# Kernel tuning notes

Measured on AMD Instinct MI355X. Metric: run time of the kernel, lower is better.

Reference implementation:

```python
import jax, jax.numpy as jnp
import numpy as np

GAIN_CAP = 0.99
EPS = 1e-4


def _clamp(v):
    # clamp_preserve_grad(v, 0.0, cap) == cap - relu(cap - relu(v))
    r = jax.nn.relu
    return GAIN_CAP - r(GAIN_CAP - r(v))


def _pos(p):
    return jax.nn.softplus(p) + EPS


def setup_inputs() -> dict:
    key = jax.random.key(0)
    ks = jax.random.split(key, 12)
    B, C, H, W, O, M = 4, 128, 256, 256, 16, 32
    return {
        "x": jax.random.normal(ks[0], (B, C, H, W), jnp.float32),
        "steer": jax.random.normal(ks[1], (B, O, H, W), jnp.float32),
        "modulation": jax.random.normal(ks[2], (B, M), jnp.float32),
        "r_center": 0.1 * jax.random.normal(ks[3], (C,), jnp.float32),
        "r_horizontal": 0.1 * jax.random.normal(ks[4], (C,), jnp.float32),
        "r_vertical": 0.1 * jax.random.normal(ks[5], (C,), jnp.float32),
        "r_diag": 0.1 * jax.random.normal(ks[6], (C,), jnp.float32),
        "gain_horizontal": 0.1 * jax.random.normal(ks[7], (C,), jnp.float32),
        "gain_vertical": 0.1 * jax.random.normal(ks[8], (C,), jnp.float32),
        "gain_diag": 0.1 * jax.random.normal(ks[9], (C,), jnp.float32),
        "steer_w": 0.1 * jax.random.normal(ks[10], (4, O), jnp.float32),  # 1x1 conv weight squeezed
        "mod_w": 0.1 * jax.random.normal(ks[11], (3, M), jnp.float32),    # Linear(M,3,bias=False)
    }


def reference(x, steer, modulation, r_center, r_horizontal, r_vertical, r_diag,
              gain_horizontal, gain_vertical, gain_diag, steer_w, mod_w):
    cview = lambda p: p[None, :, None, None]  # (1,C,1,1)
    center = x
    right = jnp.roll(x, -1, axis=-1)
    left = jnp.roll(x, 1, axis=-1)
    up = jnp.roll(x, 1, axis=-2)
    down = jnp.roll(x, -1, axis=-2)
    diag_ne = jnp.roll(x, (-1, -1), axis=(-2, -1))
    diag_sw = jnp.roll(x, (1, 1), axis=(-2, -1))
    diag_nw = jnp.roll(x, (1, -1), axis=(-2, -1))
    diag_se = jnp.roll(x, (-1, 1), axis=(-2, -1))

    r_c = cview(_pos(r_center))
    r_h = cview(_pos(r_horizontal))
    r_v = cview(_pos(r_vertical))
    r_d = cview(_pos(r_diag))

    flow_h = (right - center + (left - center)) / (r_c + r_h)
    flow_v = (up - center + (down - center)) / (r_c + r_v)
    flow_d = (diag_ne - center + (diag_sw - center) + (diag_nw - center) + (diag_se - center)) / (2.0 * (r_c + r_d))

    gh = jnp.tanh(cview(gain_horizontal))
    gv = jnp.tanh(cview(gain_vertical))
    gd = jnp.tanh(cview(gain_diag))

    # modulation gating: [B,3] -> [B,3,1,1]
    delta = jnp.tanh(modulation @ mod_w.T)[:, :, None, None]
    gh = _clamp(gh * (1.0 + 0.1 * delta[:, 0:1]))
    gv = _clamp(gv * (1.0 + 0.1 * delta[:, 1:2]))
    gd = _clamp(gd * (1.0 + 0.1 * delta[:, 2:3]))

    # steer gating: 1x1 conv (no bias) then tanh -> [B,4,H,W]
    steer_fields = jnp.tanh(jnp.einsum('bohw,po->bphw', steer, steer_w))
    gh = _clamp(gh * (1.0 + 0.2 * steer_fields[:, 0:1]))
    gv = _clamp(gv * (1.0 + 0.2 * steer_fields[:, 1:2]))
    gd = _clamp(gd * (1.0 + 0.2 * steer_fields[:, 2:3]))

    update = gh * flow_h + gv * flow_v + gd * flow_d
    return center + update
```

## Files before the change

### kernel.cpp

```cpp
#include <hip/hip_runtime.h>
#include <math.h>

#define GAIN_CAP 0.99f
#define EPSV 1e-4f

static constexpr int B = 4, C = 128, H = 256, W = 256, O = 16, M = 32;
static constexpr int HW = H * W;

typedef float vfloat4 __attribute__((ext_vector_type(4)));

static constexpr int SF_SZ = B * 3 * HW;
static constexpr int G_SZ  = B * C * 3;

__device__ __forceinline__ float softplusf(float x) {
    return log1pf(expf(-fabsf(x))) + fmaxf(x, 0.0f);
}
__device__ __forceinline__ float clampg(float v) {
    return fminf(fmaxf(v, 0.0f), GAIN_CAP);
}

__global__ void __launch_bounds__(256)
steer_kernel(const float* __restrict__ steer,
             const float* __restrict__ steer_w,
             const float* __restrict__ r_center,
             const float* __restrict__ r_h,
             const float* __restrict__ r_v,
             const float* __restrict__ r_d,
             const float* __restrict__ g_h,
             const float* __restrict__ g_v,
             const float* __restrict__ g_d,
             const float* __restrict__ modulation,
             const float* __restrict__ mod_w,
             float* __restrict__ sf,
             float* __restrict__ gains,
             float* __restrict__ invd)
{
    if (blockIdx.x == 0 && threadIdx.x < C) {
        int c = threadIdx.x;
        float rc = softplusf(r_center[c]) + EPSV;
        invd[c * 3 + 0] = 1.0f / (rc + softplusf(r_h[c]) + EPSV);
        invd[c * 3 + 1] = 1.0f / (rc + softplusf(r_v[c]) + EPSV);
        invd[c * 3 + 2] = 1.0f / (2.0f * (rc + softplusf(r_d[c]) + EPSV));
        float th = tanhf(g_h[c]), tv = tanhf(g_v[c]), td = tanhf(g_d[c]);
        for (int b = 0; b < B; ++b) {
            float a0 = 0.f, a1 = 0.f, a2 = 0.f;
#pragma unroll
            for (int m = 0; m < M; ++m) {
                float mv = modulation[b * M + m];
                a0 += mv * mod_w[0 * M + m];
                a1 += mv * mod_w[1 * M + m];
                a2 += mv * mod_w[2 * M + m];
            }
            gains[(b * C + c) * 3 + 0] = clampg(th * (1.0f + 0.1f * tanhf(a0)));
            gains[(b * C + c) * 3 + 1] = clampg(tv * (1.0f + 0.1f * tanhf(a1)));
            gains[(b * C + c) * 3 + 2] = clampg(td * (1.0f + 0.1f * tanhf(a2)));
        }
    }

    int idx = blockIdx.x * 256 + threadIdx.x;
    int b   = idx >> 14;
    int hw4 = idx & 16383;
    const float4* sp = (const float4*)(steer + ((size_t)b * O << 16)) + hw4;

    float4 a0 = {0,0,0,0}, a1 = {0,0,0,0}, a2 = {0,0,0,0};
#pragma unroll
    for (int o = 0; o < O; ++o) {
        float4 v = sp[(size_t)o << 14];
        float w0 = steer_w[o], w1 = steer_w[O + o], w2 = steer_w[2 * O + o];
        a0.x += v.x * w0; a0.y += v.y * w0; a0.z += v.z * w0; a0.w += v.w * w0;
        a1.x += v.x * w1; a1.y += v.y * w1; a1.z += v.z * w1; a1.w += v.w * w1;
        a2.x += v.x * w2; a2.y += v.y * w2; a2.z += v.z * w2; a2.w += v.w * w2;
    }
    float4* o0 = (float4*)(sf + ((size_t)(b * 3 + 0) << 16)) + hw4;
    float4* o1 = (float4*)(sf + ((size_t)(b * 3 + 1) << 16)) + hw4;
    float4* o2 = (float4*)(sf + ((size_t)(b * 3 + 2) << 16)) + hw4;
    *o0 = make_float4(tanhf(a0.x), tanhf(a0.y), tanhf(a0.z), tanhf(a0.w));
    *o1 = make_float4(tanhf(a1.x), tanhf(a1.y), tanhf(a1.z), tanhf(a1.w));
    *o2 = make_float4(tanhf(a2.x), tanhf(a2.y), tanhf(a2.z), tanhf(a2.w));
}

__global__ void __launch_bounds__(256)
main_kernel(const float* __restrict__ x,
            const float* __restrict__ sf,
            const float* __restrict__ gains,
            const float* __restrict__ invd,
            float* __restrict__ out)
{
    constexpr int RPW = 16;
    int lane  = threadIdx.x & 63;
    int wave  = threadIdx.x >> 6;
    int strip = blockIdx.x & 3;
    int bc    = blockIdx.x >> 2;
    int c     = bc & (C - 1);
    int b     = bc >> 7;
    int h0    = strip * 64 + wave * RPW;

    const float* plane = x + ((size_t)bc << 16);
    const float* sfb0  = sf + ((size_t)(b * 3 + 0) << 16);
    const float* sfb1  = sf + ((size_t)(b * 3 + 1) << 16);
    const float* sfb2  = sf + ((size_t)(b * 3 + 2) << 16);
    float*       outp  = out + ((size_t)bc << 16);

    float ih  = invd[c * 3 + 0], iv = invd[c * 3 + 1], idg = invd[c * 3 + 2];
    float g0  = gains[bc * 3 + 0], g1 = gains[bc * 3 + 1], g2 = gains[bc * 3 + 2];

    int lp = (lane + 1) & 63, lm = (lane - 1) & 63;

    float4 u4 = ((const float4*)(plane + (((h0 - 1) & 255) << 8)))[lane];
    float4 c4 = ((const float4*)(plane + (h0 << 8)))[lane];
    float uRe = __shfl(u4.x, lp), uLe = __shfl(u4.w, lm);
    float cRe = __shfl(c4.x, lp), cLe = __shfl(c4.w, lm);

    for (int r = 0; r < RPW; ++r) {
        int h  = h0 + r;
        int hd = (h + 1) & 255;
        float4 d4 = ((const float4*)(plane + (hd << 8)))[lane];
        float4 s0 = ((const float4*)(sfb0 + (h << 8)))[lane];
        float4 s1 = ((const float4*)(sfb1 + (h << 8)))[lane];
        float4 s2 = ((const float4*)(sfb2 + (h << 8)))[lane];
        float dRe = __shfl(d4.x, lp), dLe = __shfl(d4.w, lm);

        float cA[4]  = {c4.x, c4.y, c4.z, c4.w};
        float uA[4]  = {u4.x, u4.y, u4.z, u4.w};
        float dA[4]  = {d4.x, d4.y, d4.z, d4.w};
        float crA[4] = {c4.y, c4.z, c4.w, cRe};
        float clA[4] = {cLe, c4.x, c4.y, c4.z};
        float urA[4] = {u4.y, u4.z, u4.w, uRe};
        float ulA[4] = {uLe, u4.x, u4.y, u4.z};
        float drA[4] = {d4.y, d4.z, d4.w, dRe};
        float dlA[4] = {dLe, d4.x, d4.y, d4.z};
        float sA0[4] = {s0.x, s0.y, s0.z, s0.w};
        float sA1[4] = {s1.x, s1.y, s1.z, s1.w};
        float sA2[4] = {s2.x, s2.y, s2.z, s2.w};

        float oA[4];
#pragma unroll
        for (int j = 0; j < 4; ++j) {
            float fh = (crA[j] + clA[j] - 2.0f * cA[j]) * ih;
            float fv = (uA[j] + dA[j] - 2.0f * cA[j]) * iv;
            float fd = (drA[j] + dlA[j] + urA[j] + ulA[j] - 4.0f * cA[j]) * idg;
            float gh = clampg(g0 * (1.0f + 0.2f * sA0[j]));
            float gv = clampg(g1 * (1.0f + 0.2f * sA1[j]));
            float gd = clampg(g2 * (1.0f + 0.2f * sA2[j]));
            oA[j] = cA[j] + gh * fh + gv * fv + gd * fd;
        }
        vfloat4 ov = {oA[0], oA[1], oA[2], oA[3]};
        __builtin_nontemporal_store(ov, (vfloat4*)(outp + (h << 8)) + lane);

        u4 = c4; uRe = cRe; uLe = cLe;
        c4 = d4; cRe = dRe; cLe = dLe;
    }
}

extern "C" void kernel_launch(void* const* d_in, const int* in_sizes, int n_in,
                              void* d_out, int out_size, void* d_ws, size_t ws_size,
                              hipStream_t stream) {
    const float* x          = (const float*)d_in[0];
    const float* steer      = (const float*)d_in[1];
    const float* modulation = (const float*)d_in[2];
    const float* r_center   = (const float*)d_in[3];
    const float* r_horiz    = (const float*)d_in[4];
    const float* r_vert     = (const float*)d_in[5];
    const float* r_diag     = (const float*)d_in[6];
    const float* g_horiz    = (const float*)d_in[7];
    const float* g_vert     = (const float*)d_in[8];
    const float* g_diag     = (const float*)d_in[9];
    const float* steer_w    = (const float*)d_in[10];
    const float* mod_w      = (const float*)d_in[11];

    float* ws    = (float*)d_ws;
    float* sf    = ws;
    float* gains = ws + SF_SZ;
    float* invd  = gains + G_SZ;
    float* out   = (float*)d_out;

    steer_kernel<<<(B * HW / 4) / 256, 256, 0, stream>>>(
        steer, steer_w, r_center, r_horiz, r_vert, r_diag,
        g_horiz, g_vert, g_diag, modulation, mod_w, sf, gains, invd);
    main_kernel<<<B * C * 4, 256, 0, stream>>>(x, sf, gains, invd, out);
}
```

Baseline: 284.2 us.

## Pack steer fields as interleaved fp16 and process two channels per wave

The steer kernel now writes the three tanh steer fields interleaved as fp16 (padded to four halves per pixel) and uses a fast exp/rcp tanh. The main kernel handles two channels per wave with shorter row strips, so each steer-field load is shared by two channel planes and the steer traffic, which dominates the fp32 reads beyond x, is cut. In exchange it loses precision in the steer gating through fp16 and the approximate tanh, uses more registers, and spends extra halo-row reads because the strips are shorter.

```diff
diff --git a/kernel.cpp b/kernel.cpp
--- a/kernel.cpp
+++ b/kernel.cpp
@@ -7,16 +7,22 @@
 static constexpr int B = 4, C = 128, H = 256, W = 256, O = 16, M = 32;
 static constexpr int HW = H * W;
 
-typedef float vfloat4 __attribute__((ext_vector_type(4)));
-
-static constexpr int SF_SZ = B * 3 * HW;
-static constexpr int G_SZ  = B * C * 3;
+typedef float   vfloat4 __attribute__((ext_vector_type(4)));
+typedef _Float16 half4v __attribute__((ext_vector_type(4)));
+typedef _Float16 half8v __attribute__((ext_vector_type(8)));
+
+static constexpr int SFP_FLOATS = B * HW * 2;
+static constexpr int G_SZ = B * C * 3;
 
 __device__ __forceinline__ float softplusf(float x) {
     return log1pf(expf(-fabsf(x))) + fmaxf(x, 0.0f);
 }
 __device__ __forceinline__ float clampg(float v) {
     return fminf(fmaxf(v, 0.0f), GAIN_CAP);
+}
+__device__ __forceinline__ float fast_tanh(float x) {
+    float e = __expf(2.0f * x);
+    return 1.0f - 2.0f * __builtin_amdgcn_rcpf(e + 1.0f);
 }
 
 __global__ void __launch_bounds__(256)
@@ -31,7 +37,7 @@
              const float* __restrict__ g_d,
              const float* __restrict__ modulation,
              const float* __restrict__ mod_w,
-             float* __restrict__ sf,
+             half4v* __restrict__ sfp,
              float* __restrict__ gains,
              float* __restrict__ invd)
 {
@@ -58,97 +64,123 @@
     }
 
     int idx = blockIdx.x * 256 + threadIdx.x;
-    int b   = idx >> 14;
-    int hw4 = idx & 16383;
-    const float4* sp = (const float4*)(steer + ((size_t)b * O << 16)) + hw4;
-
-    float4 a0 = {0,0,0,0}, a1 = {0,0,0,0}, a2 = {0,0,0,0};
+    int b   = idx >> 16;
+    int hw  = idx & 65535;
+    const float* sp = steer + ((size_t)b * O << 16) + hw;
+
+    float a0 = 0.f, a1 = 0.f, a2 = 0.f;
 #pragma unroll
     for (int o = 0; o < O; ++o) {
-        float4 v = sp[(size_t)o << 14];
-        float w0 = steer_w[o], w1 = steer_w[O + o], w2 = steer_w[2 * O + o];
-        a0.x += v.x * w0; a0.y += v.y * w0; a0.z += v.z * w0; a0.w += v.w * w0;
-        a1.x += v.x * w1; a1.y += v.y * w1; a1.z += v.z * w1; a1.w += v.w * w1;
-        a2.x += v.x * w2; a2.y += v.y * w2; a2.z += v.z * w2; a2.w += v.w * w2;
-    }
-    float4* o0 = (float4*)(sf + ((size_t)(b * 3 + 0) << 16)) + hw4;
-    float4* o1 = (float4*)(sf + ((size_t)(b * 3 + 1) << 16)) + hw4;
-    float4* o2 = (float4*)(sf + ((size_t)(b * 3 + 2) << 16)) + hw4;
-    *o0 = make_float4(tanhf(a0.x), tanhf(a0.y), tanhf(a0.z), tanhf(a0.w));
-    *o1 = make_float4(tanhf(a1.x), tanhf(a1.y), tanhf(a1.z), tanhf(a1.w));
-    *o2 = make_float4(tanhf(a2.x), tanhf(a2.y), tanhf(a2.z), tanhf(a2.w));
+        float v = sp[(size_t)o << 16];
+        a0 += v * steer_w[o];
+        a1 += v * steer_w[O + o];
+        a2 += v * steer_w[2 * O + o];
+    }
+    half4v hv = { (_Float16)fast_tanh(a0), (_Float16)fast_tanh(a1),
+                  (_Float16)fast_tanh(a2), (_Float16)0.f };
+    sfp[idx] = hv;
+}
+
+__device__ __forceinline__ vfloat4 row_compute(
+    const float4& u, const float4& cc, const float4& d,
+    float uL, float uR, float cL, float cR, float dL, float dR,
+    float ih, float iv, float idg, float g0, float g1, float g2,
+    const float (&s0)[4], const float (&s1)[4], const float (&s2)[4])
+{
+    float cA[4]  = {cc.x, cc.y, cc.z, cc.w};
+    float uA[4]  = {u.x, u.y, u.z, u.w};
+    float dA[4]  = {d.x, d.y, d.z, d.w};
+    float crA[4] = {cc.y, cc.z, cc.w, cR};
+    float clA[4] = {cL, cc.x, cc.y, cc.z};
+    float urA[4] = {u.y, u.z, u.w, uR};
+    float ulA[4] = {uL, u.x, u.y, u.z};
+    float drA[4] = {d.y, d.z, d.w, dR};
+    float dlA[4] = {dL, d.x, d.y, d.z};
+    vfloat4 o;
+#pragma unroll
+    for (int j = 0; j < 4; ++j) {
+        float fh = (crA[j] + clA[j] - 2.0f * cA[j]) * ih;
+        float fv = (uA[j] + dA[j] - 2.0f * cA[j]) * iv;
+        float fd = (drA[j] + dlA[j] + urA[j] + ulA[j] - 4.0f * cA[j]) * idg;
+        float gh = clampg(g0 * (1.0f + 0.2f * s0[j]));
+        float gv = clampg(g1 * (1.0f + 0.2f * s1[j]));
+        float gd = clampg(g2 * (1.0f + 0.2f * s2[j]));
+        o[j] = cA[j] + gh * fh + gv * fv + gd * fd;
+    }
+    return o;
 }
 
 __global__ void __launch_bounds__(256)
 main_kernel(const float* __restrict__ x,
-            const float* __restrict__ sf,
+            const half4v* __restrict__ sfp,
             const float* __restrict__ gains,
             const float* __restrict__ invd,
             float* __restrict__ out)
 {
-    constexpr int RPW = 16;
+    constexpr int RPW = 8;
     int lane  = threadIdx.x & 63;
     int wave  = threadIdx.x >> 6;
-    int strip = blockIdx.x & 3;
-    int bc    = blockIdx.x >> 2;
-    int c     = bc & (C - 1);
-    int b     = bc >> 7;
-    int h0    = strip * 64 + wave * RPW;
-
-    const float* plane = x + ((size_t)bc << 16);
-    const float* sfb0  = sf + ((size_t)(b * 3 + 0) << 16);
-    const float* sfb1  = sf + ((size_t)(b * 3 + 1) << 16);
-    const float* sfb2  = sf + ((size_t)(b * 3 + 2) << 16);
-    float*       outp  = out + ((size_t)bc << 16);
-
-    float ih  = invd[c * 3 + 0], iv = invd[c * 3 + 1], idg = invd[c * 3 + 2];
-    float g0  = gains[bc * 3 + 0], g1 = gains[bc * 3 + 1], g2 = gains[bc * 3 + 2];
+    int gid   = blockIdx.x;
+    int strip = gid & 7;
+    int cg    = (gid >> 3) & 63;
+    int b     = gid >> 9;
+    int bc0   = b * C + cg * 2;
+    int c0    = bc0 & (C - 1);
+    int h0    = strip * 32 + wave * RPW;
+
+    const float* p0 = x + ((size_t)bc0 << 16);
+    const float* p1 = p0 + HW;
+    float* q0 = out + ((size_t)bc0 << 16);
+    float* q1 = q0 + HW;
+    const half4v* sfb = sfp + ((size_t)b << 16);
+
+    float ih0 = invd[c0 * 3 + 0], iv0 = invd[c0 * 3 + 1], id0 = invd[c0 * 3 + 2];
+    float ih1 = invd[c0 * 3 + 3], iv1 = invd[c0 * 3 + 4], id1 = invd[c0 * 3 + 5];
+    float g00 = gains[bc0 * 3 + 0], g01 = gains[bc0 * 3 + 1], g02 = gains[bc0 * 3 + 2];
+    float g10 = gains[bc0 * 3 + 3], g11 = gains[bc0 * 3 + 4], g12 = gains[bc0 * 3 + 5];
 
     int lp = (lane + 1) & 63, lm = (lane - 1) & 63;
-
-    float4 u4 = ((const float4*)(plane + (((h0 - 1) & 255) << 8)))[lane];
-    float4 c4 = ((const float4*)(plane + (h0 << 8)))[lane];
-    float uRe = __shfl(u4.x, lp), uLe = __shfl(u4.w, lm);
-    float cRe = __shfl(c4.x, lp), cLe = __shfl(c4.w, lm);
+    int hm = (h0 - 1) & 255;
+
+    float4 u0 = ((const float4*)(p0 + (hm << 8)))[lane];
+    float4 u1 = ((const float4*)(p1 + (hm << 8)))[lane];
+    float4 c0v = ((const float4*)(p0 + (h0 << 8)))[lane];
+    float4 c1v = ((const float4*)(p1 + (h0 << 8)))[lane];
+    float u0R = __shfl(u0.x, lp), u0L = __shfl(u0.w, lm);
+    float u1R = __shfl(u1.x, lp), u1L = __shfl(u1.w, lm);
+    float c0R = __shfl(c0v.x, lp), c0L = __shfl(c0v.w, lm);
+    float c1R = __shfl(c1v.x, lp), c1L = __shfl(c1v.w, lm);
 
     for (int r = 0; r < RPW; ++r) {
         int h  = h0 + r;
         int hd = (h + 1) & 255;
-        float4 d4 = ((const float4*)(plane + (hd << 8)))[lane];
-        float4 s0 = ((const float4*)(sfb0 + (h << 8)))[lane];
-        float4 s1 = ((const float4*)(sfb1 + (h << 8)))[lane];
-        float4 s2 = ((const float4*)(sfb2 + (h << 8)))[lane];
-        float dRe = __shfl(d4.x, lp), dLe = __shfl(d4.w, lm);
-
-        float cA[4]  = {c4.x, c4.y, c4.z, c4.w};
-        float uA[4]  = {u4.x, u4.y, u4.z, u4.w};
-        float dA[4]  = {d4.x, d4.y, d4.z, d4.w};
-        float crA[4] = {c4.y, c4.z, c4.w, cRe};
-        float clA[4] = {cLe, c4.x, c4.y, c4.z};
-        float urA[4] = {u4.y, u4.z, u4.w, uRe};
-        float ulA[4] = {uLe, u4.x, u4.y, u4.z};
-        float drA[4] = {d4.y, d4.z, d4.w, dRe};
-        float dlA[4] = {dLe, d4.x, d4.y, d4.z};
-        float sA0[4] = {s0.x, s0.y, s0.z, s0.w};
-        float sA1[4] = {s1.x, s1.y, s1.z, s1.w};
-        float sA2[4] = {s2.x, s2.y, s2.z, s2.w};
-
-        float oA[4];
-#pragma unroll
-        for (int j = 0; j < 4; ++j) {
-            float fh = (crA[j] + clA[j] - 2.0f * cA[j]) * ih;
-            float fv = (uA[j] + dA[j] - 2.0f * cA[j]) * iv;
-            float fd = (drA[j] + dlA[j] + urA[j] + ulA[j] - 4.0f * cA[j]) * idg;
-            float gh = clampg(g0 * (1.0f + 0.2f * sA0[j]));
-            float gv = clampg(g1 * (1.0f + 0.2f * sA1[j]));
-            float gd = clampg(g2 * (1.0f + 0.2f * sA2[j]));
-            oA[j] = cA[j] + gh * fh + gv * fv + gd * fd;
-        }
-        vfloat4 ov = {oA[0], oA[1], oA[2], oA[3]};
-        __builtin_nontemporal_store(ov, (vfloat4*)(outp + (h << 8)) + lane);
-
-        u4 = c4; uRe = cRe; uLe = cLe;
-        c4 = d4; cRe = dRe; cLe = dLe;
+        float4 d0 = ((const float4*)(p0 + (hd << 8)))[lane];
+        float4 d1 = ((const float4*)(p1 + (hd << 8)))[lane];
+        const float4* sro = (const float4*)(sfb + ((size_t)h << 8));
+        float4 sA = sro[2 * lane], sB = sro[2 * lane + 1];
+
+        float d0R = __shfl(d0.x, lp), d0L = __shfl(d0.w, lm);
+        float d1R = __shfl(d1.x, lp), d1L = __shfl(d1.w, lm);
+
+        half8v hA = __builtin_bit_cast(half8v, sA);
+        half8v hB = __builtin_bit_cast(half8v, sB);
+        float s0[4], s1[4], s2[4];
+        s0[0] = (float)hA[0]; s1[0] = (float)hA[1]; s2[0] = (float)hA[2];
+        s0[1] = (float)hA[4]; s1[1] = (float)hA[5]; s2[1] = (float)hA[6];
+        s0[2] = (float)hB[0]; s1[2] = (float)hB[1]; s2[2] = (float)hB[2];
+        s0[3] = (float)hB[4]; s1[3] = (float)hB[5]; s2[3] = (float)hB[6];
+
+        vfloat4 o0 = row_compute(u0, c0v, d0, u0L, u0R, c0L, c0R, d0L, d0R,
+                                 ih0, iv0, id0, g00, g01, g02, s0, s1, s2);
+        vfloat4 o1 = row_compute(u1, c1v, d1, u1L, u1R, c1L, c1R, d1L, d1R,
+                                 ih1, iv1, id1, g10, g11, g12, s0, s1, s2);
+        __builtin_nontemporal_store(o0, (vfloat4*)(q0 + (h << 8)) + lane);
+        __builtin_nontemporal_store(o1, (vfloat4*)(q1 + (h << 8)) + lane);
+
+        u0 = c0v; u0R = c0R; u0L = c0L;
+        u1 = c1v; u1R = c1R; u1L = c1L;
+        c0v = d0; c0R = d0R; c0L = d0L;
+        c1v = d1; c1R = d1R; c1L = d1L;
     }
 }
 
@@ -168,14 +200,14 @@
     const float* steer_w    = (const float*)d_in[10];
     const float* mod_w      = (const float*)d_in[11];
 
-    float* ws    = (float*)d_ws;
-    float* sf    = ws;
-    float* gains = ws + SF_SZ;
-    float* invd  = gains + G_SZ;
-    float* out   = (float*)d_out;
-
-    steer_kernel<<<(B * HW / 4) / 256, 256, 0, stream>>>(
+    float* ws     = (float*)d_ws;
+    half4v* sfp   = (half4v*)ws;
+    float* gains  = ws + SFP_FLOATS;
+    float* invd   = gains + G_SZ;
+    float* out    = (float*)d_out;
+
+    steer_kernel<<<(B * HW) / 256, 256, 0, stream>>>(
         steer, steer_w, r_center, r_horiz, r_vert, r_diag,
-        g_horiz, g_vert, g_diag, modulation, mod_w, sf, gains, invd);
-    main_kernel<<<B * C * 4, 256, 0, stream>>>(x, sf, gains, invd, out);
-}
+        g_horiz, g_vert, g_diag, modulation, mod_w, sfp, gains, invd);
+    main_kernel<<<B * (C / 2) * 8, 256, 0, stream>>>(x, sfp, gains, invd, out);
+}
```

Result: faster. 272.6 us (-4.1%).
